# Optimization experiments

Measured on AMD Instinct MI355X. Metric: run time of the kernel, lower is better.

The kernel has to match this reference:

```python
import jax, jax.numpy as jnp
import numpy as np

N_NODES = 50000

def setup_inputs() -> dict:
    key = jax.random.key(0)
    k1, k2, k3, k4, k5, k6 = jax.random.split(key, 6)
    T, D, N, E = 10000, 128, N_NODES, 800000
    impact = jax.random.normal(k1, (T, D), dtype=jnp.float32)
    W = jax.random.normal(k2, (D, D), dtype=jnp.float32)
    M = jax.random.normal(k3, (D, D), dtype=jnp.float32)
    node_ids = jax.random.randint(k4, (N,), 0, T, dtype=jnp.int64)
    neighbor_ids = jax.random.randint(k5, (E,), 0, T, dtype=jnp.int64)
    neighbor_segments = jnp.sort(jax.random.randint(k6, (E,), 0, N, dtype=jnp.int64))
    return {"impact": impact, "W": W, "M": M, "node_ids": node_ids,
            "neighbor_ids": neighbor_ids, "neighbor_segments": neighbor_segments}

def reference(impact, W, M, node_ids, neighbor_ids, neighbor_segments):
    # Per node i (type k_i): s_i = relu(W @ h[k_i] + sum_{j in N(i)} M @ h[type_j])
    # result = softmax(sum_i s_i) over the D feature axis.
    self_feats = impact[node_ids]                          # (N, D) gather
    neigh_feats = impact[neighbor_ids]                     # (E, D) gather
    neigh_sum = jax.ops.segment_sum(neigh_feats, neighbor_segments,
                                    num_segments=N_NODES)  # (N, D) scatter-add
    pre = self_feats @ W.T + neigh_sum @ M.T               # (N, D)
    result = jnp.sum(jax.nn.relu(pre), axis=0)             # (D,)
    return jax.nn.softmax(result, axis=0)
```

## Files before the change

kernel.cpp:

```cpp
#include <hip/hip_runtime.h>

#define DDIM 128
#define ACC_BLOCKS 2048
#define NWALK (ACC_BLOCKS * 4)
#define RED_BLOCKS 64

typedef unsigned int uint;
typedef unsigned short ushort;
typedef __attribute__((ext_vector_type(8))) short bf16x8;
typedef __attribute__((ext_vector_type(4))) float f32x4;

static __device__ __forceinline__ ushort f2bf(float x) {
    uint u = __float_as_uint(x);
    u += 0x7fffu + ((u >> 16) & 1u);
    return (ushort)(u >> 16);
}
static __device__ __forceinline__ float bflo(uint u) { return __uint_as_float(u << 16); }
static __device__ __forceinline__ float bfhi(uint u) { return __uint_as_float(u & 0xffff0000u); }

__global__ __launch_bounds__(256) void build_rowptr(
    const int* __restrict__ segs, int* __restrict__ rowptr, int* __restrict__ done,
    int N, int E)
{
    const int e = blockIdx.x * blockDim.x + threadIdx.x;
    if (e == 0) *done = 0;
    if (e >= E) return;
    const int sc = segs[e];
    const int sp = (e == 0) ? -1 : segs[e - 1];
    for (int i = sp + 1; i <= sc; ++i) rowptr[i] = e;
    if (e == E - 1) {
        for (int i = sc + 1; i <= N; ++i) rowptr[i] = E;
    }
}

__global__ __launch_bounds__(256) void build_items(
    const int* __restrict__ segs,
    const int* __restrict__ rowptr,
    const int* __restrict__ node_ids,
    const int* __restrict__ neighbor_ids,
    int* __restrict__ items,
    int* __restrict__ wstart,
    int N, int E, int whoff, int mhoff)
{
    const int x = blockIdx.x * blockDim.x + threadIdx.x;
    const int K = N + E;
    if (x < E) {
        const int s = segs[x];
        const bool last = (x + 1 == E) || (segs[x + 1] != s);
        items[x + s + 1] = (mhoff + neighbor_ids[x] * 256) | (last ? (int)0x80000000 : 0);
    }
    if (x < N) {
        const int r = rowptr[x];
        const bool last = (rowptr[x + 1] == r);
        items[r + x] = (whoff + node_ids[x] * 256) | (last ? (int)0x80000000 : 0);
    }
    if (x <= NWALK) {
        const int t = (int)(((long long)x * K) / NWALK);
        int lo = 0, hi = N;
        while (lo < hi) {
            const int mid = (lo + hi) >> 1;
            if (rowptr[mid] + mid < t) lo = mid + 1; else hi = mid;
        }
        wstart[x] = rowptr[lo] + lo;
    }
    if (x == 0) {
#pragma unroll
        for (int q = 0; q < 16; ++q) items[K + q] = whoff;
    }
}

static __device__ __forceinline__ bf16x8 load_frag8(const float* base) {
    const float4 p = *reinterpret_cast<const float4*>(base);
    const float4 q = *reinterpret_cast<const float4*>(base + 4);
    bf16x8 f;
    f[0] = (short)f2bf(p.x); f[1] = (short)f2bf(p.y);
    f[2] = (short)f2bf(p.z); f[3] = (short)f2bf(p.w);
    f[4] = (short)f2bf(q.x); f[5] = (short)f2bf(q.y);
    f[6] = (short)f2bf(q.z); f[7] = (short)f2bf(q.w);
    return f;
}

__global__ __launch_bounds__(256) void precompute_mfma(
    const float* __restrict__ impact,
    const float* __restrict__ W,
    const float* __restrict__ Mm,
    ushort* __restrict__ WhB,
    ushort* __restrict__ MhB,
    int T)
{
    const int lane = threadIdx.x & 63;
    const int wv   = threadIdx.x >> 6;
    const int t0   = blockIdx.x * 32;
    const int r16  = lane & 15;
    const int kg   = lane >> 4;

    bf16x8 A[2][4];
#pragma unroll
    for (int rt = 0; rt < 2; ++rt) {
        int t = t0 + rt * 16 + r16;
        if (t >= T) t = T - 1;
        const float* abase = impact + (size_t)t * DDIM + kg * 8;
#pragma unroll
        for (int k0i = 0; k0i < 4; ++k0i)
            A[rt][k0i] = load_frag8(abase + k0i * 32);
    }

#pragma unroll
    for (int dti = 0; dti < 2; ++dti) {
        const int d0 = (wv * 2 + dti) * 16;
#pragma unroll
        for (int m = 0; m < 2; ++m) {
            const float* mat = (m == 0) ? W : Mm;
            ushort* out = (m == 0) ? WhB : MhB;
            const float* bbase = mat + (size_t)(d0 + r16) * DDIM + kg * 8;
            f32x4 acc0 = {0.f, 0.f, 0.f, 0.f};
            f32x4 acc1 = {0.f, 0.f, 0.f, 0.f};
#pragma unroll
            for (int k0i = 0; k0i < 4; ++k0i) {
                const bf16x8 b = load_frag8(bbase + k0i * 32);
                acc0 = __builtin_amdgcn_mfma_f32_16x16x32_bf16(A[0][k0i], b, acc0, 0, 0, 0);
                acc1 = __builtin_amdgcn_mfma_f32_16x16x32_bf16(A[1][k0i], b, acc1, 0, 0, 0);
            }
            const int dcol = d0 + r16;
#pragma unroll
            for (int r = 0; r < 4; ++r) {
                const int tr0 = t0 + kg * 4 + r;
                const int tr1 = tr0 + 16;
                if (tr0 < T) out[(size_t)tr0 * DDIM + dcol] = f2bf(acc0[r]);
                if (tr1 < T) out[(size_t)tr1 * DDIM + dcol] = f2bf(acc1[r]);
            }
        }
    }
}

__global__ __launch_bounds__(256, 8) void accumulate_items(
    const char* __restrict__ tab,
    const int* __restrict__ items,
    const int* __restrict__ wstart,
    float* __restrict__ partials)
{
    const int lane = threadIdx.x & 63;
    const int wv   = __builtin_amdgcn_readfirstlane(threadIdx.x >> 6);
    const int w    = blockIdx.x * 4 + wv;

    const uint lb = (uint)lane << 2;

    float c0 = 0.f, c1 = 0.f, a0 = 0.f, a1 = 0.f;

    int k = __builtin_amdgcn_readfirstlane(wstart[w]);
    const int kend = __builtin_amdgcn_readfirstlane(wstart[w + 1]);

#define LDROW(IW) (*reinterpret_cast<const uint*>(tab + (((uint)(IW)) & 0x7fffffffu) + lb))
#define ACC(IW, V) { \
    c0 += bflo(V); c1 += bfhi(V); \
    if ((IW) < 0) { a0 += fmaxf(c0, 0.f); a1 += fmaxf(c1, 0.f); c0 = 0.f; c1 = 0.f; } }

    while (k < kend && (k & 3)) {
        const int iw = items[k];
        const uint v = LDROW(iw);
        ACC(iw, v);
        ++k;
    }
    while (k + 16 <= kend) {
        const int4 Ia = *reinterpret_cast<const int4*>(items + k);
        const int4 Ib = *reinterpret_cast<const int4*>(items + k + 4);
        const int4 Ic = *reinterpret_cast<const int4*>(items + k + 8);
        const int4 Id = *reinterpret_cast<const int4*>(items + k + 12);
        const uint v0  = LDROW(Ia.x); const uint v1  = LDROW(Ia.y);
        const uint v2  = LDROW(Ia.z); const uint v3  = LDROW(Ia.w);
        const uint v4  = LDROW(Ib.x); const uint v5  = LDROW(Ib.y);
        const uint v6  = LDROW(Ib.z); const uint v7  = LDROW(Ib.w);
        const uint v8  = LDROW(Ic.x); const uint v9  = LDROW(Ic.y);
        const uint v10 = LDROW(Ic.z); const uint v11 = LDROW(Ic.w);
        const uint v12 = LDROW(Id.x); const uint v13 = LDROW(Id.y);
        const uint v14 = LDROW(Id.z); const uint v15 = LDROW(Id.w);
        ACC(Ia.x, v0);  ACC(Ia.y, v1);  ACC(Ia.z, v2);  ACC(Ia.w, v3);
        ACC(Ib.x, v4);  ACC(Ib.y, v5);  ACC(Ib.z, v6);  ACC(Ib.w, v7);
        ACC(Ic.x, v8);  ACC(Ic.y, v9);  ACC(Ic.z, v10); ACC(Ic.w, v11);
        ACC(Id.x, v12); ACC(Id.y, v13); ACC(Id.z, v14); ACC(Id.w, v15);
        k += 16;
    }
    while (k + 4 <= kend) {
        const int4 Ia = *reinterpret_cast<const int4*>(items + k);
        const uint v0 = LDROW(Ia.x); const uint v1 = LDROW(Ia.y);
        const uint v2 = LDROW(Ia.z); const uint v3 = LDROW(Ia.w);
        ACC(Ia.x, v0); ACC(Ia.y, v1); ACC(Ia.z, v2); ACC(Ia.w, v3);
        k += 4;
    }
    while (k < kend) {
        const int iw = items[k];
        const uint v = LDROW(iw);
        ACC(iw, v);
        ++k;
    }

    a0 += fmaxf(c0, 0.f);
    a1 += fmaxf(c1, 0.f);

    __shared__ float red[4][DDIM];
    red[wv][lane * 2 + 0] = a0;
    red[wv][lane * 2 + 1] = a1;
    __syncthreads();
    const int tid = threadIdx.x;
    if (tid < DDIM) {
        partials[(size_t)blockIdx.x * DDIM + tid] =
            red[0][tid] + red[1][tid] + red[2][tid] + red[3][tid];
    }
}

__global__ __launch_bounds__(256) void reduce_softmax(
    const float* __restrict__ partials, float* __restrict__ out2,
    float* __restrict__ out, int* __restrict__ done, int nb)
{
    const int tid = threadIdx.x;
    const int d = tid & (DDIM - 1);
    const int h = tid >> 7;
    {
        const int rows = nb / RED_BLOCKS;
        const int r0 = blockIdx.x * rows;
        float s = 0.f;
        for (int r = r0 + h; r < r0 + rows; r += 2)
            s += partials[(size_t)r * DDIM + d];
        __shared__ float red[2][DDIM];
        red[h][d] = s;
        __syncthreads();
        if (tid < DDIM)
            out2[(size_t)blockIdx.x * DDIM + tid] = red[0][tid] + red[1][tid];
    }
    __threadfence();
    __shared__ int isLast;
    if (tid == 0) {
        const int v = atomicAdd(done, 1);
        isLast = (v == RED_BLOCKS - 1) ? 1 : 0;
    }
    __syncthreads();
    if (!isLast) return;
    __threadfence();

    float s = 0.f;
    for (int b = h; b < RED_BLOCKS; b += 2)
        s += out2[(size_t)b * DDIM + d];
    __shared__ float r2[2][DDIM];
    r2[h][d] = s;
    __syncthreads();

    __shared__ float vec[DDIM];
    __shared__ float tmp[DDIM];
    if (tid < DDIM) { vec[tid] = r2[0][tid] + r2[1][tid]; tmp[tid] = r2[0][tid] + r2[1][tid]; }
    __syncthreads();
    for (int o = 64; o > 0; o >>= 1) {
        if (tid < o) tmp[tid] = fmaxf(tmp[tid], tmp[tid + o]);
        __syncthreads();
    }
    const float mx = tmp[0];
    __syncthreads();
    float ev = 0.f;
    if (tid < DDIM) { ev = expf(vec[tid] - mx); tmp[tid] = ev; }
    __syncthreads();
    for (int o = 64; o > 0; o >>= 1) {
        if (tid < o) tmp[tid] += tmp[tid + o];
        __syncthreads();
    }
    if (tid < DDIM) out[tid] = ev / tmp[0];
}

extern "C" void kernel_launch(void* const* d_in, const int* in_sizes, int n_in,
                              void* d_out, int out_size, void* d_ws, size_t ws_size,
                              hipStream_t stream) {
    const float* impact        = (const float*)d_in[0];
    const float* W             = (const float*)d_in[1];
    const float* Mm            = (const float*)d_in[2];
    const int*   node_ids      = (const int*)d_in[3];
    const int*   neighbor_ids  = (const int*)d_in[4];
    const int*   neighbor_segs = (const int*)d_in[5];

    const int T = in_sizes[0] / DDIM;
    const int N = in_sizes[3];
    const int E = in_sizes[4];
    const int K = N + E;

    char* ws = (char*)d_ws;
    size_t off = 0;
    const int whoff = (int)off;
    ushort* WhB = (ushort*)(ws + off);  off += (size_t)T * DDIM * sizeof(ushort);
    const int mhoff = (int)off;
    ushort* MhB = (ushort*)(ws + off);  off += (size_t)T * DDIM * sizeof(ushort);
    float* partials = (float*)(ws + off); off += (size_t)ACC_BLOCKS * DDIM * sizeof(float);
    float* part2    = (float*)(ws + off); off += (size_t)RED_BLOCKS * DDIM * sizeof(float);
    int*   rowptr   = (int*)(ws + off);   off += (size_t)(N + 1) * sizeof(int);
    int*   done     = (int*)(ws + off);   off += 256;
    off = (off + 255) & ~(size_t)255;
    int*   items    = (int*)(ws + off);   off += (size_t)(K + 16) * sizeof(int);
    int*   wstart   = (int*)(ws + off);   off += (size_t)(NWALK + 1) * sizeof(int);
    float* outf     = (float*)d_out;

    build_rowptr<<<(E + 255) / 256, 256, 0, stream>>>(neighbor_segs, rowptr, done, N, E);
    build_items<<<(max(E, N) + 255) / 256, 256, 0, stream>>>(
        neighbor_segs, rowptr, node_ids, neighbor_ids, items, wstart, N, E, whoff, mhoff);
    precompute_mfma<<<(T + 31) / 32, 256, 0, stream>>>(impact, W, Mm, WhB, MhB, T);
    accumulate_items<<<ACC_BLOCKS, 256, 0, stream>>>(ws, items, wstart, partials);
    reduce_softmax<<<RED_BLOCKS, 256, 0, stream>>>(partials, part2, outf, done, ACC_BLOCKS);
}
```

Before: 66.04 us.

## Merge preprocessing kernels and split each wave into two half-wave walkers

Folds rowptr and item-list construction into one prep kernel, and moves the wstart binary search into the precompute kernel, cutting two launches down to one. The accumulate kernel now has each wave walk two item ranges at once, with each half-wave loading 8 bytes per lane instead of 4. Partial batches are padded with a zero row so the loop stays uniform. The aim is to reduce launch overhead and issue more gather loads per instruction, at the cost of divergent flush logic and padding reads.

```diff
diff --git a/kernel.cpp b/kernel.cpp
--- a/kernel.cpp
+++ b/kernel.cpp
@@ -2,7 +2,7 @@
 
 #define DDIM 128
 #define ACC_BLOCKS 2048
-#define NWALK (ACC_BLOCKS * 4)
+#define NHALF (ACC_BLOCKS * 4 * 2)
 #define RED_BLOCKS 64
 
 typedef unsigned int uint;
@@ -18,54 +18,38 @@
 static __device__ __forceinline__ float bflo(uint u) { return __uint_as_float(u << 16); }
 static __device__ __forceinline__ float bfhi(uint u) { return __uint_as_float(u & 0xffff0000u); }
 
-__global__ __launch_bounds__(256) void build_rowptr(
-    const int* __restrict__ segs, int* __restrict__ rowptr, int* __restrict__ done,
-    int N, int E)
-{
-    const int e = blockIdx.x * blockDim.x + threadIdx.x;
-    if (e == 0) *done = 0;
-    if (e >= E) return;
-    const int sc = segs[e];
-    const int sp = (e == 0) ? -1 : segs[e - 1];
-    for (int i = sp + 1; i <= sc; ++i) rowptr[i] = e;
-    if (e == E - 1) {
-        for (int i = sc + 1; i <= N; ++i) rowptr[i] = E;
-    }
-}
-
-__global__ __launch_bounds__(256) void build_items(
+__global__ __launch_bounds__(256) void prep(
     const int* __restrict__ segs,
-    const int* __restrict__ rowptr,
     const int* __restrict__ node_ids,
     const int* __restrict__ neighbor_ids,
+    int* __restrict__ rowptr,
     int* __restrict__ items,
-    int* __restrict__ wstart,
-    int N, int E, int whoff, int mhoff)
+    int* __restrict__ done,
+    float* __restrict__ zrow,
+    int N, int E, int whoff, int mhoff, int zpad)
 {
     const int x = blockIdx.x * blockDim.x + threadIdx.x;
-    const int K = N + E;
-    if (x < E) {
-        const int s = segs[x];
-        const bool last = (x + 1 == E) || (segs[x + 1] != s);
-        items[x + s + 1] = (mhoff + neighbor_ids[x] * 256) | (last ? (int)0x80000000 : 0);
-    }
-    if (x < N) {
-        const int r = rowptr[x];
-        const bool last = (rowptr[x + 1] == r);
-        items[r + x] = (whoff + node_ids[x] * 256) | (last ? (int)0x80000000 : 0);
-    }
-    if (x <= NWALK) {
-        const int t = (int)(((long long)x * K) / NWALK);
-        int lo = 0, hi = N;
-        while (lo < hi) {
-            const int mid = (lo + hi) >> 1;
-            if (rowptr[mid] + mid < t) lo = mid + 1; else hi = mid;
-        }
-        wstart[x] = rowptr[lo] + lo;
-    }
-    if (x == 0) {
-#pragma unroll
-        for (int q = 0; q < 16; ++q) items[K + q] = whoff;
+    if (x == 0) *done = 0;
+    if (x < 64) zrow[x] = 0.f;
+    if (x >= E) return;
+
+    const int sc = segs[x];
+    const int sp = (x == 0) ? -1 : segs[x - 1];
+    const int sn = (x + 1 < E) ? segs[x + 1] : N;
+
+    items[x + sc + 1] = (mhoff + neighbor_ids[x] * 256) | ((sn != sc) ? (int)0x80000000 : 0);
+
+    for (int i = sp + 1; i <= sc; ++i) {
+        rowptr[i] = x;
+        items[x + i] = (whoff + node_ids[i] * 256) | ((i < sc) ? (int)0x80000000 : 0);
+    }
+    if (x == E - 1) {
+        for (int i = sc + 1; i <= N; ++i) {
+            rowptr[i] = E;
+            if (i < N) items[E + i] = (whoff + node_ids[i] * 256) | (int)0x80000000;
+        }
+#pragma unroll
+        for (int q = 0; q < 16; ++q) items[N + E + q] = zpad;
     }
 }
 
@@ -86,8 +70,21 @@
     const float* __restrict__ Mm,
     ushort* __restrict__ WhB,
     ushort* __restrict__ MhB,
-    int T)
+    const int* __restrict__ rowptr,
+    int* __restrict__ wstart,
+    int T, int N, int K)
 {
+    const int gid = blockIdx.x * 256 + threadIdx.x;
+    if (gid <= NHALF) {
+        const int t = (int)(((long long)gid * K) / NHALF);
+        int lo = 0, hi = N;
+        while (lo < hi) {
+            const int mid = (lo + hi) >> 1;
+            if (rowptr[mid] + mid < t) lo = mid + 1; else hi = mid;
+        }
+        wstart[gid] = rowptr[lo] + lo;
+    }
+
     const int lane = threadIdx.x & 63;
     const int wv   = threadIdx.x >> 6;
     const int t0   = blockIdx.x * 32;
@@ -137,74 +134,74 @@
     const char* __restrict__ tab,
     const int* __restrict__ items,
     const int* __restrict__ wstart,
-    float* __restrict__ partials)
+    float* __restrict__ partials,
+    int zpad)
 {
-    const int lane = threadIdx.x & 63;
-    const int wv   = __builtin_amdgcn_readfirstlane(threadIdx.x >> 6);
+    const int tid  = threadIdx.x;
+    const int lane = tid & 63;
+    const int wv   = __builtin_amdgcn_readfirstlane(tid >> 6);
     const int w    = blockIdx.x * 4 + wv;
 
-    const uint lb = (uint)lane << 2;
-
-    float c0 = 0.f, c1 = 0.f, a0 = 0.f, a1 = 0.f;
-
-    int k = __builtin_amdgcn_readfirstlane(wstart[w]);
-    const int kend = __builtin_amdgcn_readfirstlane(wstart[w + 1]);
-
-#define LDROW(IW) (*reinterpret_cast<const uint*>(tab + (((uint)(IW)) & 0x7fffffffu) + lb))
-#define ACC(IW, V) { \
-    c0 += bflo(V); c1 += bfhi(V); \
-    if ((IW) < 0) { a0 += fmaxf(c0, 0.f); a1 += fmaxf(c1, 0.f); c0 = 0.f; c1 = 0.f; } }
-
-    while (k < kend && (k & 3)) {
-        const int iw = items[k];
-        const uint v = LDROW(iw);
-        ACC(iw, v);
-        ++k;
-    }
-    while (k + 16 <= kend) {
-        const int4 Ia = *reinterpret_cast<const int4*>(items + k);
-        const int4 Ib = *reinterpret_cast<const int4*>(items + k + 4);
-        const int4 Ic = *reinterpret_cast<const int4*>(items + k + 8);
-        const int4 Id = *reinterpret_cast<const int4*>(items + k + 12);
-        const uint v0  = LDROW(Ia.x); const uint v1  = LDROW(Ia.y);
-        const uint v2  = LDROW(Ia.z); const uint v3  = LDROW(Ia.w);
-        const uint v4  = LDROW(Ib.x); const uint v5  = LDROW(Ib.y);
-        const uint v6  = LDROW(Ib.z); const uint v7  = LDROW(Ib.w);
-        const uint v8  = LDROW(Ic.x); const uint v9  = LDROW(Ic.y);
-        const uint v10 = LDROW(Ic.z); const uint v11 = LDROW(Ic.w);
-        const uint v12 = LDROW(Id.x); const uint v13 = LDROW(Id.y);
-        const uint v14 = LDROW(Id.z); const uint v15 = LDROW(Id.w);
-        ACC(Ia.x, v0);  ACC(Ia.y, v1);  ACC(Ia.z, v2);  ACC(Ia.w, v3);
-        ACC(Ib.x, v4);  ACC(Ib.y, v5);  ACC(Ib.z, v6);  ACC(Ib.w, v7);
-        ACC(Ic.x, v8);  ACC(Ic.y, v9);  ACC(Ic.z, v10); ACC(Ic.w, v11);
-        ACC(Id.x, v12); ACC(Id.y, v13); ACC(Id.z, v14); ACC(Id.w, v15);
-        k += 16;
-    }
-    while (k + 4 <= kend) {
-        const int4 Ia = *reinterpret_cast<const int4*>(items + k);
-        const uint v0 = LDROW(Ia.x); const uint v1 = LDROW(Ia.y);
-        const uint v2 = LDROW(Ia.z); const uint v3 = LDROW(Ia.w);
-        ACC(Ia.x, v0); ACC(Ia.y, v1); ACC(Ia.z, v2); ACC(Ia.w, v3);
-        k += 4;
-    }
-    while (k < kend) {
-        const int iw = items[k];
-        const uint v = LDROW(iw);
-        ACC(iw, v);
-        ++k;
-    }
-
-    a0 += fmaxf(c0, 0.f);
-    a1 += fmaxf(c1, 0.f);
-
-    __shared__ float red[4][DDIM];
-    red[wv][lane * 2 + 0] = a0;
-    red[wv][lane * 2 + 1] = a1;
-    __syncthreads();
-    const int tid = threadIdx.x;
+    int kA        = __builtin_amdgcn_readfirstlane(wstart[2 * w]);
+    const int kAe = __builtin_amdgcn_readfirstlane(wstart[2 * w + 1]);
+    int kB        = kAe;
+    const int kBe = __builtin_amdgcn_readfirstlane(wstart[2 * w + 2]);
+
+    const bool isB  = lane >= 32;
+    const uint vbase = (uint)(lane & 31) * 8u;
+
+    float c0 = 0.f, c1 = 0.f, c2 = 0.f, c3 = 0.f;
+    float a0 = 0.f, a1 = 0.f, a2 = 0.f, a3 = 0.f;
+
+    while (kA < kAe || kB < kBe) {
+        int wA[8], wB[8];
+        if (kA + 8 <= kAe && kB + 8 <= kBe) {
+#pragma unroll
+            for (int j = 0; j < 8; ++j) { wA[j] = items[kA + j]; wB[j] = items[kB + j]; }
+        } else {
+#pragma unroll
+            for (int j = 0; j < 8; ++j) {
+                wA[j] = (kA + j < kAe) ? items[kA + j] : zpad;
+                wB[j] = (kB + j < kBe) ? items[kB + j] : zpad;
+            }
+        }
+        uint2 v[8];
+#pragma unroll
+        for (int j = 0; j < 8; ++j) {
+            const uint off = ((uint)(isB ? wB[j] : wA[j]) & 0x7fffffffu) + vbase;
+            v[j] = *reinterpret_cast<const uint2*>(tab + off);
+        }
+#pragma unroll
+        for (int j = 0; j < 8; ++j) {
+            c0 += bflo(v[j].x); c1 += bfhi(v[j].x);
+            c2 += bflo(v[j].y); c3 += bfhi(v[j].y);
+            const bool fA = wA[j] < 0;
+            const bool fB = wB[j] < 0;
+            if (__builtin_amdgcn_ballot_w64(1) && (fA || fB)) {
+                const bool myf = isB ? fB : fA;
+                a0 += myf ? fmaxf(c0, 0.f) : 0.f;
+                a1 += myf ? fmaxf(c1, 0.f) : 0.f;
+                a2 += myf ? fmaxf(c2, 0.f) : 0.f;
+                a3 += myf ? fmaxf(c3, 0.f) : 0.f;
+                c0 = myf ? 0.f : c0;  c1 = myf ? 0.f : c1;
+                c2 = myf ? 0.f : c2;  c3 = myf ? 0.f : c3;
+            }
+        }
+        kA = min(kA + 8, kAe);
+        kB = min(kB + 8, kBe);
+    }
+    a0 += fmaxf(c0, 0.f); a1 += fmaxf(c1, 0.f);
+    a2 += fmaxf(c2, 0.f); a3 += fmaxf(c3, 0.f);
+
+    __shared__ float red[8][DDIM];
+    *reinterpret_cast<float4*>(&red[wv * 2 + (isB ? 1 : 0)][(lane & 31) * 4]) =
+        make_float4(a0, a1, a2, a3);
+    __syncthreads();
     if (tid < DDIM) {
-        partials[(size_t)blockIdx.x * DDIM + tid] =
-            red[0][tid] + red[1][tid] + red[2][tid] + red[3][tid];
+        float s = 0.f;
+#pragma unroll
+        for (int g = 0; g < 8; ++g) s += red[g][tid];
+        partials[(size_t)blockIdx.x * DDIM + tid] = s;
     }
 }
 
@@ -246,7 +243,7 @@
 
     __shared__ float vec[DDIM];
     __shared__ float tmp[DDIM];
-    if (tid < DDIM) { vec[tid] = r2[0][tid] + r2[1][tid]; tmp[tid] = r2[0][tid] + r2[1][tid]; }
+    if (tid < DDIM) { const float v = r2[0][tid] + r2[1][tid]; vec[tid] = v; tmp[tid] = v; }
     __syncthreads();
     for (int o = 64; o > 0; o >>= 1) {
         if (tid < o) tmp[tid] = fmaxf(tmp[tid], tmp[tid + o]);
@@ -285,19 +282,22 @@
     ushort* WhB = (ushort*)(ws + off);  off += (size_t)T * DDIM * sizeof(ushort);
     const int mhoff = (int)off;
     ushort* MhB = (ushort*)(ws + off);  off += (size_t)T * DDIM * sizeof(ushort);
+    const int zoff = (int)off;
+    float* zrow = (float*)(ws + off);   off += 64 * sizeof(float);
     float* partials = (float*)(ws + off); off += (size_t)ACC_BLOCKS * DDIM * sizeof(float);
     float* part2    = (float*)(ws + off); off += (size_t)RED_BLOCKS * DDIM * sizeof(float);
     int*   rowptr   = (int*)(ws + off);   off += (size_t)(N + 1) * sizeof(int);
     int*   done     = (int*)(ws + off);   off += 256;
     off = (off + 255) & ~(size_t)255;
     int*   items    = (int*)(ws + off);   off += (size_t)(K + 16) * sizeof(int);
-    int*   wstart   = (int*)(ws + off);   off += (size_t)(NWALK + 1) * sizeof(int);
+    int*   wstart   = (int*)(ws + off);   off += (size_t)(NHALF + 1) * sizeof(int);
     float* outf     = (float*)d_out;
 
-    build_rowptr<<<(E + 255) / 256, 256, 0, stream>>>(neighbor_segs, rowptr, done, N, E);
-    build_items<<<(max(E, N) + 255) / 256, 256, 0, stream>>>(
-        neighbor_segs, rowptr, node_ids, neighbor_ids, items, wstart, N, E, whoff, mhoff);
-    precompute_mfma<<<(T + 31) / 32, 256, 0, stream>>>(impact, W, Mm, WhB, MhB, T);
-    accumulate_items<<<ACC_BLOCKS, 256, 0, stream>>>(ws, items, wstart, partials);
+    prep<<<(E + 255) / 256, 256, 0, stream>>>(
+        neighbor_segs, node_ids, neighbor_ids, rowptr, items, done, zrow,
+        N, E, whoff, mhoff, zoff);
+    precompute_mfma<<<(T + 31) / 32, 256, 0, stream>>>(
+        impact, W, Mm, WhB, MhB, rowptr, wstart, T, N, K);
+    accumulate_items<<<ACC_BLOCKS, 256, 0, stream>>>(ws, items, wstart, partials, zoff);
     reduce_softmax<<<RED_BLOCKS, 256, 0, stream>>>(partials, part2, outf, done, ACC_BLOCKS);
 }
```

Result: slower. 71.01 us (+7.5%).

## Store projected tables in fp32 and fold preprocessing kernels into fewer launches

Applied to the files above, without the earlier changes.

The W·h and M·h lookup tables are now stored as fp32 instead of bf16, and the gather loop reads a float2 per lane instead of a packed bf16 pair. The rowptr and items building is merged into one kernel. The wstart binary search moves into the MFMA precompute kernel, which removes one launch and one dependent pass. This saves a launch and the bf16 pack/unpack work and improves accuracy, but it doubles the bytes each gathered row costs in the dominant accumulate kernel.

```diff
diff --git a/kernel.cpp b/kernel.cpp
--- a/kernel.cpp
+++ b/kernel.cpp
@@ -15,57 +15,37 @@
     u += 0x7fffu + ((u >> 16) & 1u);
     return (ushort)(u >> 16);
 }
-static __device__ __forceinline__ float bflo(uint u) { return __uint_as_float(u << 16); }
-static __device__ __forceinline__ float bfhi(uint u) { return __uint_as_float(u & 0xffff0000u); }
-
-__global__ __launch_bounds__(256) void build_rowptr(
-    const int* __restrict__ segs, int* __restrict__ rowptr, int* __restrict__ done,
-    int N, int E)
-{
-    const int e = blockIdx.x * blockDim.x + threadIdx.x;
-    if (e == 0) *done = 0;
-    if (e >= E) return;
-    const int sc = segs[e];
-    const int sp = (e == 0) ? -1 : segs[e - 1];
-    for (int i = sp + 1; i <= sc; ++i) rowptr[i] = e;
-    if (e == E - 1) {
-        for (int i = sc + 1; i <= N; ++i) rowptr[i] = E;
-    }
-}
-
-__global__ __launch_bounds__(256) void build_items(
+
+__global__ __launch_bounds__(256) void prep(
     const int* __restrict__ segs,
-    const int* __restrict__ rowptr,
     const int* __restrict__ node_ids,
     const int* __restrict__ neighbor_ids,
+    int* __restrict__ rowptr,
     int* __restrict__ items,
-    int* __restrict__ wstart,
+    int* __restrict__ done,
     int N, int E, int whoff, int mhoff)
 {
     const int x = blockIdx.x * blockDim.x + threadIdx.x;
-    const int K = N + E;
-    if (x < E) {
-        const int s = segs[x];
-        const bool last = (x + 1 == E) || (segs[x + 1] != s);
-        items[x + s + 1] = (mhoff + neighbor_ids[x] * 256) | (last ? (int)0x80000000 : 0);
-    }
-    if (x < N) {
-        const int r = rowptr[x];
-        const bool last = (rowptr[x + 1] == r);
-        items[r + x] = (whoff + node_ids[x] * 256) | (last ? (int)0x80000000 : 0);
-    }
-    if (x <= NWALK) {
-        const int t = (int)(((long long)x * K) / NWALK);
-        int lo = 0, hi = N;
-        while (lo < hi) {
-            const int mid = (lo + hi) >> 1;
-            if (rowptr[mid] + mid < t) lo = mid + 1; else hi = mid;
+    if (x == 0) *done = 0;
+    if (x >= E) return;
+
+    const int sc = segs[x];
+    const int sp = (x == 0) ? -1 : segs[x - 1];
+    const int sn = (x + 1 < E) ? segs[x + 1] : N;
+
+    items[x + sc + 1] = (mhoff + neighbor_ids[x] * 512) | ((sn != sc) ? (int)0x80000000 : 0);
+
+    for (int i = sp + 1; i <= sc; ++i) {
+        rowptr[i] = x;
+        items[x + i] = (whoff + node_ids[i] * 512) | ((i < sc) ? (int)0x80000000 : 0);
+    }
+    if (x == E - 1) {
+        for (int i = sc + 1; i <= N; ++i) {
+            rowptr[i] = E;
+            if (i < N) items[E + i] = (whoff + node_ids[i] * 512) | (int)0x80000000;
         }
-        wstart[x] = rowptr[lo] + lo;
-    }
-    if (x == 0) {
-#pragma unroll
-        for (int q = 0; q < 16; ++q) items[K + q] = whoff;
+#pragma unroll
+        for (int q = 0; q < 16; ++q) items[N + E + q] = whoff;
     }
 }
 
@@ -84,10 +64,23 @@
     const float* __restrict__ impact,
     const float* __restrict__ W,
     const float* __restrict__ Mm,
-    ushort* __restrict__ WhB,
-    ushort* __restrict__ MhB,
-    int T)
-{
+    float* __restrict__ WhF,
+    float* __restrict__ MhF,
+    const int* __restrict__ rowptr,
+    int* __restrict__ wstart,
+    int T, int N, int K)
+{
+    const int gid = blockIdx.x * 256 + threadIdx.x;
+    if (gid <= NWALK) {
+        const int t = (int)(((long long)gid * K) / NWALK);
+        int lo = 0, hi = N;
+        while (lo < hi) {
+            const int mid = (lo + hi) >> 1;
+            if (rowptr[mid] + mid < t) lo = mid + 1; else hi = mid;
+        }
+        wstart[gid] = rowptr[lo] + lo;
+    }
+
     const int lane = threadIdx.x & 63;
     const int wv   = threadIdx.x >> 6;
     const int t0   = blockIdx.x * 32;
@@ -111,7 +104,7 @@
 #pragma unroll
         for (int m = 0; m < 2; ++m) {
             const float* mat = (m == 0) ? W : Mm;
-            ushort* out = (m == 0) ? WhB : MhB;
+            float* out = (m == 0) ? WhF : MhF;
             const float* bbase = mat + (size_t)(d0 + r16) * DDIM + kg * 8;
             f32x4 acc0 = {0.f, 0.f, 0.f, 0.f};
             f32x4 acc1 = {0.f, 0.f, 0.f, 0.f};
@@ -126,8 +119,8 @@
             for (int r = 0; r < 4; ++r) {
                 const int tr0 = t0 + kg * 4 + r;
                 const int tr1 = tr0 + 16;
-                if (tr0 < T) out[(size_t)tr0 * DDIM + dcol] = f2bf(acc0[r]);
-                if (tr1 < T) out[(size_t)tr1 * DDIM + dcol] = f2bf(acc1[r]);
+                if (tr0 < T) out[(size_t)tr0 * DDIM + dcol] = acc0[r];
+                if (tr1 < T) out[(size_t)tr1 * DDIM + dcol] = acc1[r];
             }
         }
     }
@@ -143,21 +136,21 @@
     const int wv   = __builtin_amdgcn_readfirstlane(threadIdx.x >> 6);
     const int w    = blockIdx.x * 4 + wv;
 
-    const uint lb = (uint)lane << 2;
+    const uint lb = (uint)lane << 3;
 
     float c0 = 0.f, c1 = 0.f, a0 = 0.f, a1 = 0.f;
 
     int k = __builtin_amdgcn_readfirstlane(wstart[w]);
     const int kend = __builtin_amdgcn_readfirstlane(wstart[w + 1]);
 
-#define LDROW(IW) (*reinterpret_cast<const uint*>(tab + (((uint)(IW)) & 0x7fffffffu) + lb))
+#define LDROW(IW) (*reinterpret_cast<const float2*>(tab + (((uint)(IW)) & 0x7fffffffu) + lb))
 #define ACC(IW, V) { \
-    c0 += bflo(V); c1 += bfhi(V); \
+    c0 += (V).x; c1 += (V).y; \
     if ((IW) < 0) { a0 += fmaxf(c0, 0.f); a1 += fmaxf(c1, 0.f); c0 = 0.f; c1 = 0.f; } }
 
     while (k < kend && (k & 3)) {
         const int iw = items[k];
-        const uint v = LDROW(iw);
+        const float2 v = LDROW(iw);
         ACC(iw, v);
         ++k;
     }
@@ -166,14 +159,14 @@
         const int4 Ib = *reinterpret_cast<const int4*>(items + k + 4);
         const int4 Ic = *reinterpret_cast<const int4*>(items + k + 8);
         const int4 Id = *reinterpret_cast<const int4*>(items + k + 12);
-        const uint v0  = LDROW(Ia.x); const uint v1  = LDROW(Ia.y);
-        const uint v2  = LDROW(Ia.z); const uint v3  = LDROW(Ia.w);
-        const uint v4  = LDROW(Ib.x); const uint v5  = LDROW(Ib.y);
-        const uint v6  = LDROW(Ib.z); const uint v7  = LDROW(Ib.w);
-        const uint v8  = LDROW(Ic.x); const uint v9  = LDROW(Ic.y);
-        const uint v10 = LDROW(Ic.z); const uint v11 = LDROW(Ic.w);
-        const uint v12 = LDROW(Id.x); const uint v13 = LDROW(Id.y);
-        const uint v14 = LDROW(Id.z); const uint v15 = LDROW(Id.w);
+        const float2 v0  = LDROW(Ia.x); const float2 v1  = LDROW(Ia.y);
+        const float2 v2  = LDROW(Ia.z); const float2 v3  = LDROW(Ia.w);
+        const float2 v4  = LDROW(Ib.x); const float2 v5  = LDROW(Ib.y);
+        const float2 v6  = LDROW(Ib.z); const float2 v7  = LDROW(Ib.w);
+        const float2 v8  = LDROW(Ic.x); const float2 v9  = LDROW(Ic.y);
+        const float2 v10 = LDROW(Ic.z); const float2 v11 = LDROW(Ic.w);
+        const float2 v12 = LDROW(Id.x); const float2 v13 = LDROW(Id.y);
+        const float2 v14 = LDROW(Id.z); const float2 v15 = LDROW(Id.w);
         ACC(Ia.x, v0);  ACC(Ia.y, v1);  ACC(Ia.z, v2);  ACC(Ia.w, v3);
         ACC(Ib.x, v4);  ACC(Ib.y, v5);  ACC(Ib.z, v6);  ACC(Ib.w, v7);
         ACC(Ic.x, v8);  ACC(Ic.y, v9);  ACC(Ic.z, v10); ACC(Ic.w, v11);
@@ -182,14 +175,14 @@
     }
     while (k + 4 <= kend) {
         const int4 Ia = *reinterpret_cast<const int4*>(items + k);
-        const uint v0 = LDROW(Ia.x); const uint v1 = LDROW(Ia.y);
-        const uint v2 = LDROW(Ia.z); const uint v3 = LDROW(Ia.w);
+        const float2 v0 = LDROW(Ia.x); const float2 v1 = LDROW(Ia.y);
+        const float2 v2 = LDROW(Ia.z); const float2 v3 = LDROW(Ia.w);
         ACC(Ia.x, v0); ACC(Ia.y, v1); ACC(Ia.z, v2); ACC(Ia.w, v3);
         k += 4;
     }
     while (k < kend) {
         const int iw = items[k];
-        const uint v = LDROW(iw);
+        const float2 v = LDROW(iw);
         ACC(iw, v);
         ++k;
     }
@@ -246,7 +239,7 @@
 
     __shared__ float vec[DDIM];
     __shared__ float tmp[DDIM];
-    if (tid < DDIM) { vec[tid] = r2[0][tid] + r2[1][tid]; tmp[tid] = r2[0][tid] + r2[1][tid]; }
+    if (tid < DDIM) { const float v = r2[0][tid] + r2[1][tid]; vec[tid] = v; tmp[tid] = v; }
     __syncthreads();
     for (int o = 64; o > 0; o >>= 1) {
         if (tid < o) tmp[tid] = fmaxf(tmp[tid], tmp[tid + o]);
@@ -282,9 +275,9 @@
     char* ws = (char*)d_ws;
     size_t off = 0;
     const int whoff = (int)off;
-    ushort* WhB = (ushort*)(ws + off);  off += (size_t)T * DDIM * sizeof(ushort);
+    float* WhF = (float*)(ws + off);    off += (size_t)T * DDIM * sizeof(float);
     const int mhoff = (int)off;
-    ushort* MhB = (ushort*)(ws + off);  off += (size_t)T * DDIM * sizeof(ushort);
+    float* MhF = (float*)(ws + off);    off += (size_t)T * DDIM * sizeof(float);
     float* partials = (float*)(ws + off); off += (size_t)ACC_BLOCKS * DDIM * sizeof(float);
     float* part2    = (float*)(ws + off); off += (size_t)RED_BLOCKS * DDIM * sizeof(float);
     int*   rowptr   = (int*)(ws + off);   off += (size_t)(N + 1) * sizeof(int);
@@ -294,10 +287,10 @@
     int*   wstart   = (int*)(ws + off);   off += (size_t)(NWALK + 1) * sizeof(int);
     float* outf     = (float*)d_out;
 
-    build_rowptr<<<(E + 255) / 256, 256, 0, stream>>>(neighbor_segs, rowptr, done, N, E);
-    build_items<<<(max(E, N) + 255) / 256, 256, 0, stream>>>(
-        neighbor_segs, rowptr, node_ids, neighbor_ids, items, wstart, N, E, whoff, mhoff);
-    precompute_mfma<<<(T + 31) / 32, 256, 0, stream>>>(impact, W, Mm, WhB, MhB, T);
+    prep<<<(E + 255) / 256, 256, 0, stream>>>(
+        neighbor_segs, node_ids, neighbor_ids, rowptr, items, done, N, E, whoff, mhoff);
+    precompute_mfma<<<(T + 31) / 32, 256, 0, stream>>>(
+        impact, W, Mm, WhF, MhF, rowptr, wstart, T, N, K);
     accumulate_items<<<ACC_BLOCKS, 256, 0, stream>>>(ws, items, wstart, partials);
     reduce_softmax<<<RED_BLOCKS, 256, 0, stream>>>(partials, part2, outf, done, ACC_BLOCKS);
 }
```

Measured after the change: 77.62 us. 1.18x slower.
